# Kernel tuning notes

Measured on AMD Instinct MI355X. Metric: run time of the kernel, lower is better.

The kernel has to match this reference:

```python
import jax, jax.numpy as jnp
import numpy as np

B, SQ, SK, D, DV = 8, 2048, 4096, 512, 256

def setup_inputs() -> dict:
    key = jax.random.key(0)
    k1, k2, k3, k4, k5 = jax.random.split(key, 5)
    X = jax.random.normal(k1, (B, SQ, D), dtype=jnp.float32)
    Y = jax.random.normal(k2, (SK, D), dtype=jnp.float32)
    Z = jax.random.normal(k3, (SK, D), dtype=jnp.float32)
    # Linear weights (torch stores [out, in]); scaled like default init
    W_k = jax.random.normal(k4, (D, D), dtype=jnp.float32) / np.sqrt(D)
    W_v = jax.random.normal(k5, (DV, D), dtype=jnp.float32) / np.sqrt(D)
    return {"X": X, "Y": Y, "Z": Z, "W_k": W_k, "W_v": W_v, "rate": 0}


def reference(X, Y, Z, W_k, W_v, rate):
    # key = W_k(Y).unsqueeze(0): [1, SK, D]; value = W_v(Z).unsqueeze(0): [1, SK, DV]
    key = (Y @ W_k.T)[None]
    value = (Z @ W_v.T)[None]
    # scores = X @ key^T / sqrt(d): [B, SQ, SK] (key batch dim broadcasts)
    scale = 1.0 / jnp.sqrt(jnp.asarray(X.shape[-1], dtype=X.dtype))
    scores = jnp.matmul(X, jnp.swapaxes(key, 1, 2)) * scale
    attn = jax.nn.softmax(scores, axis=-1)
    # dropout layers act as identity in eval mode
    out = jnp.matmul(attn, value)  # [B, SQ, DV]
    return out
```

## Files before the change

### kernel.cpp

```cpp
#include <hip/hip_runtime.h>
#include <hip/hip_bf16.h>

#define NB    8
#define SQN   2048
#define SKN   4096
#define DDIM  512
#define DVDIM 256
#define NROWS (NB*SQN)
#define NS    2
#define NJ    ((SKN/64)/NS)

typedef __attribute__((ext_vector_type(8))) short bf16x8;
typedef __attribute__((ext_vector_type(4))) short bf16x4;
typedef __attribute__((ext_vector_type(4))) float f32x4;

__device__ __forceinline__ short f2bf(float f) {
    unsigned u = __float_as_uint(f);
    return (short)((u + 0x7FFFu + ((u >> 16) & 1u)) >> 16);
}

__device__ __forceinline__ void gload_lds16(const void* g, void* l) {
    __builtin_amdgcn_global_load_lds(
        (const __attribute__((address_space(1))) unsigned int*)g,
        (__attribute__((address_space(3))) unsigned int*)l, 16, 0, 0);
}

__global__ __launch_bounds__(256, 2) void proj_gemms(
    const float* __restrict__ Y, const float* __restrict__ Z,
    const float* __restrict__ Wk, const float* __restrict__ Wv,
    unsigned short* __restrict__ keyb, unsigned short* __restrict__ vtb)
{
    __shared__ short sA[64*128];
    __shared__ short sB[64*128];
    const float *A, *Bm;
    unsigned short* C;
    int N, m0, n0;
    if (blockIdx.z == 0) {
        A = Y; Bm = Wk; C = keyb; N = DDIM;
        m0 = blockIdx.x * 64; n0 = blockIdx.y * 64;
    } else {
        int lin = blockIdx.x * 8 + blockIdx.y;
        if (lin >= 256) return;
        A = Wv; Bm = Z; C = vtb; N = SKN;
        m0 = (lin >> 6) * 64; n0 = (lin & 63) * 64;
    }
    const int tid  = threadIdx.x;
    const int wave = tid >> 6;
    const int lane = tid & 63;
    const int quad = lane >> 4;
    const int l15  = lane & 15;

    f32x4 acc[4];
    #pragma unroll
    for (int n = 0; n < 4; ++n) { acc[n][0]=0.f; acc[n][1]=0.f; acc[n][2]=0.f; acc[n][3]=0.f; }

    float4 ra[8], rb[8];
    #pragma unroll
    for (int it = 0; it < 8; ++it) {
        int f = it*1024 + tid*4, row = f >> 7, col = f & 127;
        ra[it] = *(const float4*)(A  + (size_t)(m0+row)*DDIM + col);
        rb[it] = *(const float4*)(Bm + (size_t)(n0+row)*DDIM + col);
    }

    for (int kc = 0; kc < DDIM; kc += 128) {
        __syncthreads();
        #pragma unroll
        for (int it = 0; it < 8; ++it) {
            int f = it*1024 + tid*4;
            bf16x4 a4; a4[0]=f2bf(ra[it].x); a4[1]=f2bf(ra[it].y); a4[2]=f2bf(ra[it].z); a4[3]=f2bf(ra[it].w);
            *(bf16x4*)(sA + f) = a4;
            bf16x4 b4; b4[0]=f2bf(rb[it].x); b4[1]=f2bf(rb[it].y); b4[2]=f2bf(rb[it].z); b4[3]=f2bf(rb[it].w);
            *(bf16x4*)(sB + f) = b4;
        }
        __syncthreads();
        if (kc + 128 < DDIM) {
            #pragma unroll
            for (int it = 0; it < 8; ++it) {
                int f = it*1024 + tid*4, row = f >> 7, col = f & 127;
                ra[it] = *(const float4*)(A  + (size_t)(m0+row)*DDIM + kc + 128 + col);
                rb[it] = *(const float4*)(Bm + (size_t)(n0+row)*DDIM + kc + 128 + col);
            }
        }
        #pragma unroll
        for (int t = 0; t < 4; ++t) {
            bf16x8 af = *(const bf16x8*)(sA + (wave*16 + l15)*128 + t*32 + quad*8);
            #pragma unroll
            for (int n = 0; n < 4; ++n) {
                bf16x8 bfr = *(const bf16x8*)(sB + (n*16 + l15)*128 + t*32 + quad*8);
                acc[n] = __builtin_amdgcn_mfma_f32_16x16x32_bf16(af, bfr, acc[n], 0, 0, 0);
            }
        }
    }
    #pragma unroll
    for (int n = 0; n < 4; ++n)
        #pragma unroll
        for (int r = 0; r < 4; ++r) {
            int m  = m0 + wave*16 + quad*4 + r;
            int nn = n0 + n*16 + l15;
            C[(size_t)m*N + nn] = (unsigned short)f2bf(acc[n][r]);
        }
}

__global__ __launch_bounds__(256, 2) void attn_fused(
    const float* __restrict__ X,
    const unsigned short* __restrict__ Kb,
    const unsigned short* __restrict__ Vt,
    float* __restrict__ Opart,
    float* __restrict__ Mpart,
    float* __restrict__ Lpart)
{
    __shared__ short sK[2][8192];
    __shared__ short sV[16384];
    __shared__ short sP[4096];
    const int tid  = threadIdx.x;
    const int wave = tid >> 6;
    const int lane = tid & 63;
    const int quad = lane >> 4;
    const int l15  = lane & 15;
    const int l7   = lane & 7;
    const int split = blockIdx.y;
    const int q0   = blockIdx.x * 64;
    const int sb0  = split * NJ;
    const float scale = 0.04419417382415922f;

    bf16x8 qf[16];
    {
        const float* xrow = X + (size_t)(q0 + wave*16 + l15) * DDIM;
        #pragma unroll
        for (int t = 0; t < 16; ++t) {
            float4 a = *(const float4*)(xrow + t*32 + quad*8);
            float4 b = *(const float4*)(xrow + t*32 + quad*8 + 4);
            bf16x8 q;
            q[0]=f2bf(a.x*scale); q[1]=f2bf(a.y*scale); q[2]=f2bf(a.z*scale); q[3]=f2bf(a.w*scale);
            q[4]=f2bf(b.x*scale); q[5]=f2bf(b.y*scale); q[6]=f2bf(b.z*scale); q[7]=f2bf(b.w*scale);
            qf[t] = q;
        }
    }

    f32x4 o[16];
    #pragma unroll
    for (int i = 0; i < 16; ++i) { o[i][0]=0.f; o[i][1]=0.f; o[i][2]=0.f; o[i][3]=0.f; }
    float m_r[4] = {-1e30f,-1e30f,-1e30f,-1e30f};
    float l_r[4] = {0.f,0.f,0.f,0.f};
    short* sPw = sP + wave*1024;

    const int wq   = wave*4 + quad;
    const int vrow = wave*8 + (lane>>3);
    const int vswz = (l7 ^ (lane>>3)) << 3;

    #define STAGE_K(sk0_, c_, buf_)                                            \
        do {                                                                   \
            const unsigned short* ksrc_ = Kb + (size_t)((sk0_) + wq)*DDIM      \
                + (c_)*128 + ((l15 ^ wq) << 3);                                \
            char* kdst_ = (char*)(buf_) + wave*1024;                           \
            _Pragma("unroll")                                                  \
            for (int it_ = 0; it_ < 4; ++it_)                                  \
                gload_lds16(ksrc_ + (size_t)it_*16*DDIM, kdst_ + it_*4096);    \
        } while (0)

    STAGE_K(sb0*64, 0, sK[0]);

    for (int j = 0; j < NJ; ++j) {
        const int sk0 = (sb0 + j) * 64;
        f32x4 s[4];
        #pragma unroll
        for (int n = 0; n < 4; ++n) { s[n][0]=0.f; s[n][1]=0.f; s[n][2]=0.f; s[n][3]=0.f; }

        #pragma unroll
        for (int c = 0; c < 4; ++c) {
            __syncthreads();
            if (c == 0) {
                const unsigned short* vsrc = Vt + sk0 + (size_t)vrow*SKN + vswz;
                char* vdst = (char*)sV + wave*1024;
                #pragma unroll
                for (int it = 0; it < 8; ++it)
                    gload_lds16(vsrc + (size_t)it*32*SKN, vdst + it*4096);
            }
            if (c < 3)            STAGE_K(sk0,      c + 1, sK[(c + 1) & 1]);
            else if (j + 1 < NJ)  STAGE_K(sk0 + 64, 0,     sK[0]);
            const short* sKc = sK[c & 1];
            #pragma unroll
            for (int t = 0; t < 4; ++t) {
                bf16x8 af = qf[c*4 + t];
                #pragma unroll
                for (int n = 0; n < 4; ++n) {
                    bf16x8 bfr = *(const bf16x8*)(sKc + (n*16 + l15)*128
                                                  + (((t*4 + quad) ^ l15) << 3));
                    s[n] = __builtin_amdgcn_mfma_f32_16x16x32_bf16(af, bfr, s[n], 0, 0, 0);
                }
            }
        }

        float alpha[4];
        int need_rescale = 0;
        #pragma unroll
        for (int r = 0; r < 4; ++r) {
            float v = fmaxf(fmaxf(s[0][r], s[1][r]), fmaxf(s[2][r], s[3][r]));
            v = fmaxf(v, __shfl_xor(v, 1));
            v = fmaxf(v, __shfl_xor(v, 2));
            v = fmaxf(v, __shfl_xor(v, 4));
            v = fmaxf(v, __shfl_xor(v, 8));
            float mn = fmaxf(m_r[r], v);
            float a  = __expf(m_r[r] - mn);
            alpha[r] = a;
            need_rescale |= (a < 1.0f);
            m_r[r] = mn;
            const int row = quad*4 + r;
            short* prow = sPw + row*64 + l7;
            const int rx = row & 7;
            float sum = 0.f;
            #pragma unroll
            for (int n = 0; n < 4; ++n) {
                float pv = __expf(s[n][r] - mn);
                sum += pv;
                prow[((n*2 + (l15 >> 3)) ^ rx) << 3] = f2bf(pv);
            }
            sum += __shfl_xor(sum, 1);
            sum += __shfl_xor(sum, 2);
            sum += __shfl_xor(sum, 4);
            sum += __shfl_xor(sum, 8);
            l_r[r] = l_r[r]*a + sum;
        }
        if (__any(need_rescale)) {
            #pragma unroll
            for (int n2 = 0; n2 < 16; ++n2)
                #pragma unroll
                for (int r = 0; r < 4; ++r) o[n2][r] *= alpha[r];
        }

        #pragma unroll
        for (int t2 = 0; t2 < 2; ++t2) {
            const int cx = (((t2*4 + quad) ^ l7) << 3);
            bf16x8 af = *(const bf16x8*)(sPw + l15*64 + cx);
            #pragma unroll
            for (int n2 = 0; n2 < 16; ++n2) {
                bf16x8 bfr = *(const bf16x8*)(sV + (n2*16 + l15)*64 + cx);
                o[n2] = __builtin_amdgcn_mfma_f32_16x16x32_bf16(af, bfr, o[n2], 0, 0, 0);
            }
        }
    }
    #undef STAGE_K

    const size_t base = (size_t)split * NROWS;
    #pragma unroll
    for (int r = 0; r < 4; ++r) {
        int row = q0 + wave*16 + quad*4 + r;
        if (l15 == 0) { Mpart[base + row] = m_r[r]; Lpart[base + row] = l_r[r]; }
        float* orow = Opart + (base + row) * (size_t)DVDIM;
        #pragma unroll
        for (int n2 = 0; n2 < 16; ++n2)
            orow[n2*16 + l15] = o[n2][r];
    }
}

__global__ void combine_splits(
    const float* __restrict__ Opart, const float* __restrict__ Mpart,
    const float* __restrict__ Lpart, float* __restrict__ out)
{
    const int row = blockIdx.x * 4 + (threadIdx.x >> 6);
    const int dv4 = (threadIdx.x & 63) * 4;
    float M = -1e30f;
    #pragma unroll
    for (int s = 0; s < NS; ++s) M = fmaxf(M, Mpart[(size_t)s*NROWS + row]);
    float denom = 0.f;
    float4 acc = make_float4(0.f, 0.f, 0.f, 0.f);
    #pragma unroll
    for (int s = 0; s < NS; ++s) {
        float w = __expf(Mpart[(size_t)s*NROWS + row] - M);
        denom += Lpart[(size_t)s*NROWS + row] * w;
        float4 ov = *(const float4*)(Opart + ((size_t)s*NROWS + row)*DVDIM + dv4);
        acc.x += ov.x*w; acc.y += ov.y*w; acc.z += ov.z*w; acc.w += ov.w*w;
    }
    float inv = 1.0f / denom;
    *(float4*)(out + (size_t)row*DVDIM + dv4)
        = make_float4(acc.x*inv, acc.y*inv, acc.z*inv, acc.w*inv);
}

extern "C" void kernel_launch(void* const* d_in, const int* in_sizes, int n_in,
                              void* d_out, int out_size, void* d_ws, size_t ws_size,
                              hipStream_t stream) {
    const float* X  = (const float*)d_in[0];
    const float* Y  = (const float*)d_in[1];
    const float* Z  = (const float*)d_in[2];
    const float* Wk = (const float*)d_in[3];
    const float* Wv = (const float*)d_in[4];
    float* out = (float*)d_out;

    char* ws = (char*)d_ws;
    unsigned short* keyb = (unsigned short*)ws;
    unsigned short* vtb  = (unsigned short*)(ws + (4u<<20));
    float* Opart = (float*)(ws + (6u<<20));
    float* Mpart = (float*)(ws + (6u<<20) + (size_t)NS*NROWS*DVDIM*4);
    float* Lpart = Mpart + (size_t)NS*NROWS;

    proj_gemms<<<dim3(64, 8, 2), dim3(256), 0, stream>>>(Y, Z, Wk, Wv, keyb, vtb);
    attn_fused<<<dim3(NROWS/64, NS), dim3(256), 0, stream>>>(
        X, keyb, vtb, Opart, Mpart, Lpart);
    combine_splits<<<dim3(NROWS/4), dim3(256), 0, stream>>>(Opart, Mpart, Lpart, out);
}
```

Baseline: 299.1 us.

## Switch attention to 32x32x16 MFMA with register-resident P and in-block KV split

Rewrites the fused attention kernel to use 32x32x16 bf16 MFMAs, computing S^T so the softmax probabilities stay in registers. Packing uses v_cvt_pk_bf16_f32 and v_permlane32_swap instead of a round trip through shared memory. Waves are split 2x2 over query rows and key halves of each tile, and the two key halves are merged with a shared-memory reduction at the end. This is meant to cut LDS traffic and MFMA instruction count, at the cost of more registers (32 Q fragments, 128 accumulator floats) and an extra end-of-kernel combine step.

```diff
diff --git a/kernel.cpp b/kernel.cpp
--- a/kernel.cpp
+++ b/kernel.cpp
@@ -10,9 +10,10 @@
 #define NS    2
 #define NJ    ((SKN/64)/NS)
 
-typedef __attribute__((ext_vector_type(8))) short bf16x8;
-typedef __attribute__((ext_vector_type(4))) short bf16x4;
-typedef __attribute__((ext_vector_type(4))) float f32x4;
+typedef __attribute__((ext_vector_type(8)))  short bf16x8;
+typedef __attribute__((ext_vector_type(4)))  short bf16x4;
+typedef __attribute__((ext_vector_type(4)))  float f32x4;
+typedef __attribute__((ext_vector_type(16))) float f32x16;
 
 __device__ __forceinline__ short f2bf(float f) {
     unsigned u = __float_as_uint(f);
@@ -109,27 +110,30 @@
     float* __restrict__ Mpart,
     float* __restrict__ Lpart)
 {
-    __shared__ short sK[2][8192];
-    __shared__ short sV[16384];
-    __shared__ short sP[4096];
+    __shared__ __align__(16) char smem[66560];
+    short* sK0 = (short*)smem;
+    short* sK1 = (short*)(smem + 16384);
+    short* sVs = (short*)(smem + 32768);
+    float* sSt = (float*)(smem + 65536);
+
     const int tid  = threadIdx.x;
     const int wave = tid >> 6;
     const int lane = tid & 63;
-    const int quad = lane >> 4;
-    const int l15  = lane & 15;
-    const int l7   = lane & 7;
+    const int l31  = lane & 31;
+    const int hi   = lane >> 5;
+    const int wm   = wave >> 1;
+    const int wk   = wave & 1;
     const int split = blockIdx.y;
     const int q0   = blockIdx.x * 64;
-    const int sb0  = split * NJ;
     const float scale = 0.04419417382415922f;
 
-    bf16x8 qf[16];
+    bf16x8 qf[32];
     {
-        const float* xrow = X + (size_t)(q0 + wave*16 + l15) * DDIM;
-        #pragma unroll
-        for (int t = 0; t < 16; ++t) {
-            float4 a = *(const float4*)(xrow + t*32 + quad*8);
-            float4 b = *(const float4*)(xrow + t*32 + quad*8 + 4);
+        const float* xrow = X + (size_t)(q0 + wm*32 + l31)*DDIM + hi*8;
+        #pragma unroll
+        for (int t = 0; t < 32; ++t) {
+            float4 a = *(const float4*)(xrow + t*16);
+            float4 b = *(const float4*)(xrow + t*16 + 4);
             bf16x8 q;
             q[0]=f2bf(a.x*scale); q[1]=f2bf(a.y*scale); q[2]=f2bf(a.z*scale); q[3]=f2bf(a.w*scale);
             q[4]=f2bf(b.x*scale); q[5]=f2bf(b.y*scale); q[6]=f2bf(b.z*scale); q[7]=f2bf(b.w*scale);
@@ -137,119 +141,154 @@
         }
     }
 
-    f32x4 o[16];
-    #pragma unroll
-    for (int i = 0; i < 16; ++i) { o[i][0]=0.f; o[i][1]=0.f; o[i][2]=0.f; o[i][3]=0.f; }
-    float m_r[4] = {-1e30f,-1e30f,-1e30f,-1e30f};
-    float l_r[4] = {0.f,0.f,0.f,0.f};
-    short* sPw = sP + wave*1024;
-
-    const int wq   = wave*4 + quad;
-    const int vrow = wave*8 + (lane>>3);
-    const int vswz = (l7 ^ (lane>>3)) << 3;
-
-    #define STAGE_K(sk0_, c_, buf_)                                            \
-        do {                                                                   \
-            const unsigned short* ksrc_ = Kb + (size_t)((sk0_) + wq)*DDIM      \
-                + (c_)*128 + ((l15 ^ wq) << 3);                                \
-            char* kdst_ = (char*)(buf_) + wave*1024;                           \
-            _Pragma("unroll")                                                  \
-            for (int it_ = 0; it_ < 4; ++it_)                                  \
-                gload_lds16(ksrc_ + (size_t)it_*16*DDIM, kdst_ + it_*4096);    \
+    f32x16 o[8];
+    #pragma unroll
+    for (int n = 0; n < 8; ++n)
+        #pragma unroll
+        for (int r = 0; r < 16; ++r) o[n][r] = 0.f;
+    float m_r = -1e30f, l_r = 0.f;
+
+    const int jt0 = split * (NJ*64);
+
+    #define STAGE_K(jtb_, cc_, buf_)                                          \
+        do {                                                                  \
+            _Pragma("unroll")                                                 \
+            for (int it_ = 0; it_ < 4; ++it_) {                               \
+                int row_ = wave*16 + it_*4 + (lane>>4);                       \
+                const char* src_ = (const char*)Kb                            \
+                    + (size_t)((jtb_) + row_)*1024 + (cc_)*256                \
+                    + (((lane&15) ^ (row_&15)) << 4);                         \
+                gload_lds16(src_, (char*)(buf_) + wave*4096 + it_*1024);      \
+            }                                                                 \
         } while (0)
 
-    STAGE_K(sb0*64, 0, sK[0]);
+    #define STAGE_V(jtb_)                                                     \
+        do {                                                                  \
+            _Pragma("unroll")                                                 \
+            for (int it_ = 0; it_ < 8; ++it_) {                               \
+                int dv_ = wave*64 + it_*8 + (lane>>3);                        \
+                const char* src_ = (const char*)Vt + (size_t)dv_*8192         \
+                    + (size_t)(jtb_)*2 + (((lane&7) ^ (lane>>3)) << 4);       \
+                gload_lds16(src_, (char*)sVs + wave*8192 + it_*1024);         \
+            }                                                                 \
+        } while (0)
+
+    STAGE_K(jt0, 0, sK0);
+
+    const int krow = wk*32 + l31;
+    const int kswz = (krow & 15) << 3;
 
     for (int j = 0; j < NJ; ++j) {
-        const int sk0 = (sb0 + j) * 64;
-        f32x4 s[4];
-        #pragma unroll
-        for (int n = 0; n < 4; ++n) { s[n][0]=0.f; s[n][1]=0.f; s[n][2]=0.f; s[n][3]=0.f; }
+        const int jtb = jt0 + j*64;
+        f32x16 s;
+        #pragma unroll
+        for (int r = 0; r < 16; ++r) s[r] = 0.f;
 
         #pragma unroll
         for (int c = 0; c < 4; ++c) {
             __syncthreads();
-            if (c == 0) {
-                const unsigned short* vsrc = Vt + sk0 + (size_t)vrow*SKN + vswz;
-                char* vdst = (char*)sV + wave*1024;
+            if (c == 0) STAGE_V(jtb);
+            if (c < 3)            STAGE_K(jtb,    c+1, (c&1) ? sK0 : sK1);
+            else if (j+1 < NJ)    STAGE_K(jtb+64, 0,   sK0);
+            const short* sKc = (c&1) ? sK1 : sK0;
+            const short* krb = sKc + krow*128;
+            #pragma unroll
+            for (int t = 0; t < 8; ++t) {
+                bf16x8 kf = *(const bf16x8*)(krb + ((t*16 + hi*8) ^ kswz));
+                s = __builtin_amdgcn_mfma_f32_32x32x16_bf16(kf, qf[c*8+t], s, 0, 0, 0);
+            }
+        }
+
+        float tmax = s[0];
+        #pragma unroll
+        for (int r = 1; r < 16; ++r) tmax = fmaxf(tmax, s[r]);
+        tmax = fmaxf(tmax, __shfl_xor(tmax, 32));
+        float mn = fmaxf(m_r, tmax);
+        float alpha = __expf(m_r - mn);
+        float p[16]; float tsum = 0.f;
+        #pragma unroll
+        for (int r = 0; r < 16; ++r) { p[r] = __expf(s[r] - mn); tsum += p[r]; }
+        tsum += __shfl_xor(tsum, 32);
+        l_r = l_r * alpha + tsum;
+        m_r = mn;
+        if (__any(alpha < 1.f)) {
+            #pragma unroll
+            for (int r = 0; r < 16; ++r) {
+                int row = (r&3) + 8*(r>>2) + 4*hi;
+                float ar = __shfl(alpha, row);
                 #pragma unroll
-                for (int it = 0; it < 8; ++it)
-                    gload_lds16(vsrc + (size_t)it*32*SKN, vdst + it*4096);
-            }
-            if (c < 3)            STAGE_K(sk0,      c + 1, sK[(c + 1) & 1]);
-            else if (j + 1 < NJ)  STAGE_K(sk0 + 64, 0,     sK[0]);
-            const short* sKc = sK[c & 1];
-            #pragma unroll
-            for (int t = 0; t < 4; ++t) {
-                bf16x8 af = qf[c*4 + t];
-                #pragma unroll
-                for (int n = 0; n < 4; ++n) {
-                    bf16x8 bfr = *(const bf16x8*)(sKc + (n*16 + l15)*128
-                                                  + (((t*4 + quad) ^ l15) << 3));
-                    s[n] = __builtin_amdgcn_mfma_f32_16x16x32_bf16(af, bfr, s[n], 0, 0, 0);
-                }
-            }
-        }
-
-        float alpha[4];
-        int need_rescale = 0;
-        #pragma unroll
-        for (int r = 0; r < 4; ++r) {
-            float v = fmaxf(fmaxf(s[0][r], s[1][r]), fmaxf(s[2][r], s[3][r]));
-            v = fmaxf(v, __shfl_xor(v, 1));
-            v = fmaxf(v, __shfl_xor(v, 2));
-            v = fmaxf(v, __shfl_xor(v, 4));
-            v = fmaxf(v, __shfl_xor(v, 8));
-            float mn = fmaxf(m_r[r], v);
-            float a  = __expf(m_r[r] - mn);
-            alpha[r] = a;
-            need_rescale |= (a < 1.0f);
-            m_r[r] = mn;
-            const int row = quad*4 + r;
-            short* prow = sPw + row*64 + l7;
-            const int rx = row & 7;
-            float sum = 0.f;
-            #pragma unroll
-            for (int n = 0; n < 4; ++n) {
-                float pv = __expf(s[n][r] - mn);
-                sum += pv;
-                prow[((n*2 + (l15 >> 3)) ^ rx) << 3] = f2bf(pv);
-            }
-            sum += __shfl_xor(sum, 1);
-            sum += __shfl_xor(sum, 2);
-            sum += __shfl_xor(sum, 4);
-            sum += __shfl_xor(sum, 8);
-            l_r[r] = l_r[r]*a + sum;
-        }
-        if (__any(need_rescale)) {
-            #pragma unroll
-            for (int n2 = 0; n2 < 16; ++n2)
-                #pragma unroll
-                for (int r = 0; r < 4; ++r) o[n2][r] *= alpha[r];
-        }
-
-        #pragma unroll
-        for (int t2 = 0; t2 < 2; ++t2) {
-            const int cx = (((t2*4 + quad) ^ l7) << 3);
-            bf16x8 af = *(const bf16x8*)(sPw + l15*64 + cx);
-            #pragma unroll
-            for (int n2 = 0; n2 < 16; ++n2) {
-                bf16x8 bfr = *(const bf16x8*)(sV + (n2*16 + l15)*64 + cx);
-                o[n2] = __builtin_amdgcn_mfma_f32_16x16x32_bf16(af, bfr, o[n2], 0, 0, 0);
-            }
-        }
+                for (int n = 0; n < 8; ++n) o[n][r] *= ar;
+            }
+        }
+
+        bf16x8 pf[2];
+        #pragma unroll
+        for (int ks = 0; ks < 2; ++ks) {
+            int wA, wB, wC, wD;
+            asm("v_cvt_pk_bf16_f32 %0, %1, %2" : "=v"(wA) : "v"(p[8*ks+0]), "v"(p[8*ks+1]));
+            asm("v_cvt_pk_bf16_f32 %0, %1, %2" : "=v"(wB) : "v"(p[8*ks+2]), "v"(p[8*ks+3]));
+            asm("v_cvt_pk_bf16_f32 %0, %1, %2" : "=v"(wC) : "v"(p[8*ks+4]), "v"(p[8*ks+5]));
+            asm("v_cvt_pk_bf16_f32 %0, %1, %2" : "=v"(wD) : "v"(p[8*ks+6]), "v"(p[8*ks+7]));
+            asm("v_permlane32_swap_b32 %0, %1" : "+v"(wA), "+v"(wC));
+            asm("v_permlane32_swap_b32 %0, %1" : "+v"(wB), "+v"(wD));
+            union { int w[4]; bf16x8 v; } u;
+            u.w[0] = wA; u.w[1] = wB; u.w[2] = wC; u.w[3] = wD;
+            pf[ks] = u.v;
+        }
+
+        #pragma unroll
+        for (int ks = 0; ks < 2; ++ks)
+            #pragma unroll
+            for (int n = 0; n < 8; ++n) {
+                int dv = n*32 + l31;
+                bf16x8 vf = *(const bf16x8*)(sVs + dv*64
+                                + ((wk*32 + ks*16 + hi*8) ^ ((dv&7)<<3)));
+                o[n] = __builtin_amdgcn_mfma_f32_32x32x16_bf16(pf[ks], vf, o[n], 0, 0, 0);
+            }
     }
     #undef STAGE_K
-
-    const size_t base = (size_t)split * NROWS;
-    #pragma unroll
-    for (int r = 0; r < 4; ++r) {
-        int row = q0 + wave*16 + quad*4 + r;
-        if (l15 == 0) { Mpart[base + row] = m_r[r]; Lpart[base + row] = l_r[r]; }
-        float* orow = Opart + (base + row) * (size_t)DVDIM;
-        #pragma unroll
-        for (int n2 = 0; n2 < 16; ++n2)
-            orow[n2*16 + l15] = o[n2][r];
+    #undef STAGE_V
+
+    __syncthreads();
+    if (lane < 32) {
+        sSt[((wm*2+wk)*2+0)*32 + lane] = m_r;
+        sSt[((wm*2+wk)*2+1)*32 + lane] = l_r;
+    }
+    __syncthreads();
+    float* obuf = (float*)(smem + wm*32768);
+    if (wk == 1) {
+        #pragma unroll
+        for (int n = 0; n < 8; ++n)
+            #pragma unroll
+            for (int r = 0; r < 16; ++r) {
+                int row = (r&3) + 8*(r>>2) + 4*hi;
+                obuf[row*256 + n*32 + l31] = o[n][r];
+            }
+    }
+    __syncthreads();
+    if (wk == 0) {
+        float m0 = sSt[((wm*2+0)*2+0)*32 + l31];
+        float m1 = sSt[((wm*2+1)*2+0)*32 + l31];
+        float l0 = sSt[((wm*2+0)*2+1)*32 + l31];
+        float l1 = sSt[((wm*2+1)*2+1)*32 + l31];
+        float M  = fmaxf(m0, m1);
+        float w0 = __expf(m0 - M), w1 = __expf(m1 - M);
+        const size_t base = (size_t)split * NROWS;
+        const int gr0 = q0 + wm*32;
+        if (lane < 32) {
+            Mpart[base + gr0 + lane] = M;
+            Lpart[base + gr0 + lane] = l0*w0 + l1*w1;
+        }
+        #pragma unroll
+        for (int r = 0; r < 16; ++r) {
+            int row = (r&3) + 8*(r>>2) + 4*hi;
+            float w0r = __shfl(w0, row);
+            float w1r = __shfl(w1, row);
+            float* orow = Opart + (base + gr0 + row) * (size_t)DVDIM;
+            #pragma unroll
+            for (int n = 0; n < 8; ++n)
+                orow[n*32 + l31] = o[n][r]*w0r + obuf[row*256 + n*32 + l31]*w1r;
+        }
     }
 }
 
```

After: 399.4 us. 1.34x slower.
